# Optimization experiments

Hardware: AMD Instinct MI355X
Metric: run time of the kernel (lower is better)

Reference implementation:

```python
import jax, jax.numpy as jnp
import numpy as np

EMBED_DIM = 1024
NUM_HEADS = 16
HEAD_DIM = EMBED_DIM // NUM_HEADS


def setup_inputs() -> dict:
    key = jax.random.key(0)
    ks = jax.random.split(key, 9)
    B, S, D = 2, 2048, EMBED_DIM
    scale = 1.0 / np.sqrt(D)
    x = jax.random.normal(ks[0], (B, S, D), dtype=jnp.float32)
    Wq = jax.random.normal(ks[1], (D, D), dtype=jnp.float32) * scale
    Wk = jax.random.normal(ks[2], (D, D), dtype=jnp.float32) * scale
    Wv = jax.random.normal(ks[3], (D, D), dtype=jnp.float32) * scale
    Wo = jax.random.normal(ks[4], (D, D), dtype=jnp.float32) * scale
    bq = jnp.zeros((D,), jnp.float32)
    bk = jnp.zeros((D,), jnp.float32)
    bv = jnp.zeros((D,), jnp.float32)
    bo = jnp.zeros((D,), jnp.float32)
    return {"x": x, "Wq": Wq, "bq": bq, "Wk": Wk, "bk": bk,
            "Wv": Wv, "bv": bv, "Wo": Wo, "bo": bo}


def reference(x, Wq, bq, Wk, bk, Wv, bv, Wo, bo):
    B, S, D = x.shape
    H, Dh = NUM_HEADS, HEAD_DIM
    # QKV projections -> [B, H, S, Dh]
    q = (x @ Wq + bq).reshape(B, S, H, Dh).transpose(0, 2, 1, 3)
    k = (x @ Wk + bk).reshape(B, S, H, Dh).transpose(0, 2, 1, 3)
    v = (x @ Wv + bv).reshape(B, S, H, Dh).transpose(0, 2, 1, 3)
    # scores [B, H, S, S], scaled by sqrt(head_dim)
    scores = jnp.einsum('bhqd,bhkd->bhqk', q, k) / jnp.sqrt(jnp.float32(Dh))
    attn = jax.nn.softmax(scores, axis=-1)
    out = jnp.einsum('bhqk,bhkd->bhqd', attn, v)  # [B, H, S, Dh]
    out = out.transpose(0, 2, 1, 3).reshape(B, S, D)
    return out @ Wo + bo
```

## Files before the change

kernel.cpp:

```cpp
#include <hip/hip_runtime.h>
#include <hip/hip_bf16.h>

typedef short bf16x8 __attribute__((ext_vector_type(8)));
typedef float f32x4 __attribute__((ext_vector_type(4)));
typedef unsigned uint2v __attribute__((ext_vector_type(2)));

#define MFMA16(a, b, c) __builtin_amdgcn_mfma_f32_16x16x32_bf16((a), (b), (c), 0, 0, 0)

#if __has_builtin(__builtin_amdgcn_exp2f)
#define EXP2(x) __builtin_amdgcn_exp2f(x)
#else
#define EXP2(x) exp2f(x)
#endif

static constexpr int B_ = 2, S_ = 2048, D_ = 1024, H_ = 16, DH = 64;
static constexpr int M_ = B_ * S_;
static constexpr int K_ = D_;
static constexpr float kQS = 0.18033688011112042f;

static __device__ __forceinline__ ushort f2bf(float f) {
    __hip_bfloat16 h = __float2bfloat16(f);
    return *reinterpret_cast<ushort*>(&h);
}
static __device__ __forceinline__ float bf2f(ushort u) {
    __hip_bfloat16 h;
    *reinterpret_cast<ushort*>(&h) = u;
    return __bfloat162float(h);
}

static __device__ __forceinline__ void gload16(const ushort* g, ushort* l) {
    __builtin_amdgcn_global_load_lds((const __attribute__((address_space(1))) void*)g,
                                     (__attribute__((address_space(3))) void*)l, 16, 0, 0);
}

static __device__ __forceinline__ unsigned pkbf(float lo, float hi) {
    return __builtin_amdgcn_perm(__builtin_bit_cast(unsigned, hi),
                                 __builtin_bit_cast(unsigned, lo), 0x07060302u);
}

__global__ __launch_bounds__(256) void prep5(const float* __restrict__ x,
                                             const float* __restrict__ W0,
                                             const float* __restrict__ W1,
                                             const float* __restrict__ W2,
                                             const float* __restrict__ W3,
                                             ushort* __restrict__ xb,
                                             ushort* __restrict__ T0,
                                             ushort* __restrict__ T1,
                                             ushort* __restrict__ T2,
                                             ushort* __restrict__ T3) {
    int z = blockIdx.z;
    int tx = threadIdx.x, ty = threadIdx.y;
    int t = ty * 32 + tx;
    if (z == 4) {
        int blk = blockIdx.y * 32 + blockIdx.x;
#pragma unroll
        for (int k = 0; k < 4; k++) {
            int i = blk * 1024 + k * 256 + t;
            float4 v = reinterpret_cast<const float4*>(x)[i];
            ushort4 o;
            o.x = f2bf(v.x); o.y = f2bf(v.y); o.z = f2bf(v.z); o.w = f2bf(v.w);
            reinterpret_cast<ushort4*>(xb)[i] = o;
        }
        return;
    }
    __shared__ float tile[32][33];
    const float* W = (z == 0) ? W0 : (z == 1) ? W1 : (z == 2) ? W2 : W3;
    ushort* T = (z == 0) ? T0 : (z == 1) ? T1 : (z == 2) ? T2 : T3;
    float sc = (z == 0) ? kQS : 1.0f;
    int bx = blockIdx.x, by = blockIdx.y;
#pragma unroll
    for (int i = 0; i < 4; i++)
        tile[ty + i * 8][tx] = W[(by * 32 + ty + i * 8) * D_ + bx * 32 + tx];
    __syncthreads();
#pragma unroll
    for (int i = 0; i < 4; i++)
        T[(bx * 32 + ty + i * 8) * K_ + by * 32 + tx] = f2bf(tile[tx][ty + i * 8] * sc);
}

template <int MODE, int TN>
__global__ __launch_bounds__(256, 3) void gemm128(const ushort* __restrict__ A,
                                                  const ushort* __restrict__ Wt,
                                                  const float* __restrict__ bias_q,
                                                  const float* __restrict__ bias_k,
                                                  const float* __restrict__ bias_v,
                                                  ushort* __restrict__ Qb,
                                                  ushort* __restrict__ Kb,
                                                  ushort* __restrict__ Vtb,
                                                  float* __restrict__ outf) {
    constexpr int NJ = TN / 32;
    __shared__ __align__(16) ushort As[128 * 32];
    __shared__ __align__(16) ushort Bs[TN * 32];

    int m0 = blockIdx.x * 128;
    int n0 = blockIdx.y * TN;
    int t = threadIdx.x;
    int lane = t & 63, w = t >> 6;
    int ln = lane & 15, lq = lane >> 4;
    int wm = (w >> 1) * 64, wn = (w & 1) * (TN / 2);

    int c0 = t, c1 = t + 256;
    const ushort* Ag0 = A + (size_t)(m0 + (c0 >> 2)) * K_ + (c0 & 3) * 8;
    const ushort* Ag1 = A + (size_t)(m0 + (c1 >> 2)) * K_ + (c1 & 3) * 8;
    const ushort* Bg0 = Wt + (size_t)(n0 + (c0 >> 2)) * K_ + (c0 & 3) * 8;
    const ushort* Bg1 = Wt + (size_t)(n0 + (c1 >> 2)) * K_ + (c1 & 3) * 8;
    ushort* Al0 = As + c0 * 8;
    ushort* Al1 = As + c1 * 8;
    ushort* Bl0 = Bs + c0 * 8;
    ushort* Bl1 = Bs + c1 * 8;

    const bool swp = (MODE == 1) || (n0 < 2048);

    f32x4 acc[4][NJ];
#pragma unroll
    for (int i = 0; i < 4; i++)
#pragma unroll
        for (int j = 0; j < NJ; j++) acc[i][j] = f32x4{0.f, 0.f, 0.f, 0.f};

    if (swp) {
        for (int k0 = 0; k0 < K_; k0 += 32) {
            gload16(Ag0 + k0, Al0);
            gload16(Ag1 + k0, Al1);
            gload16(Bg0 + k0, Bl0);
            if (TN == 128) gload16(Bg1 + k0, Bl1);
            __syncthreads();
            bf16x8 af[4], bfr[NJ];
#pragma unroll
            for (int i = 0; i < 4; i++)
                af[i] = *reinterpret_cast<const bf16x8*>(As + (wm + i * 16 + ln) * 32 + lq * 8);
#pragma unroll
            for (int j = 0; j < NJ; j++)
                bfr[j] = *reinterpret_cast<const bf16x8*>(Bs + (wn + j * 16 + ln) * 32 + lq * 8);
#pragma unroll
            for (int i = 0; i < 4; i++)
#pragma unroll
                for (int j = 0; j < NJ; j++)
                    acc[i][j] = MFMA16(bfr[j], af[i], acc[i][j]);
            __syncthreads();
        }
    } else {
        for (int k0 = 0; k0 < K_; k0 += 32) {
            gload16(Ag0 + k0, Al0);
            gload16(Ag1 + k0, Al1);
            gload16(Bg0 + k0, Bl0);
            if (TN == 128) gload16(Bg1 + k0, Bl1);
            __syncthreads();
            bf16x8 af[4], bfr[NJ];
#pragma unroll
            for (int i = 0; i < 4; i++)
                af[i] = *reinterpret_cast<const bf16x8*>(As + (wm + i * 16 + ln) * 32 + lq * 8);
#pragma unroll
            for (int j = 0; j < NJ; j++)
                bfr[j] = *reinterpret_cast<const bf16x8*>(Bs + (wn + j * 16 + ln) * 32 + lq * 8);
#pragma unroll
            for (int i = 0; i < 4; i++)
#pragma unroll
                for (int j = 0; j < NJ; j++)
                    acc[i][j] = MFMA16(af[i], bfr[j], acc[i][j]);
            __syncthreads();
        }
    }

    if (MODE == 1) {
#pragma unroll
        for (int j = 0; j < NJ; j++) {
            int nb = n0 + wn + j * 16 + lq * 4;
            float4 bv4 = *reinterpret_cast<const float4*>(bias_q + nb);
#pragma unroll
            for (int i = 0; i < 4; i++) {
                int m = m0 + wm + i * 16 + ln;
                float4 o;
                o.x = acc[i][j][0] + bv4.x;
                o.y = acc[i][j][1] + bv4.y;
                o.z = acc[i][j][2] + bv4.z;
                o.w = acc[i][j][3] + bv4.w;
                *reinterpret_cast<float4*>(outf + (size_t)m * D_ + nb) = o;
            }
        }
    } else if (n0 < 2048) {
        int which = n0 >> 10;
        const float* bp = which ? bias_k : bias_q;
        ushort* dst = which ? Kb : Qb;
        float bsc = which ? 1.0f : kQS;
#pragma unroll
        for (int j = 0; j < NJ; j++) {
            int nb = ((n0 + wn + j * 16) & 1023) + lq * 4;
            int h = nb >> 6, dhb = nb & 63;
            float4 bv4 = *reinterpret_cast<const float4*>(bp + nb);
            bv4.x *= bsc; bv4.y *= bsc; bv4.z *= bsc; bv4.w *= bsc;
#pragma unroll
            for (int i = 0; i < 4; i++) {
                int m = m0 + wm + i * 16 + ln;
                int b = m >> 11, s = m & 2047;
                ushort4 o4;
                o4.x = f2bf(acc[i][j][0] + bv4.x);
                o4.y = f2bf(acc[i][j][1] + bv4.y);
                o4.z = f2bf(acc[i][j][2] + bv4.z);
                o4.w = f2bf(acc[i][j][3] + bv4.w);
                *reinterpret_cast<ushort4*>(dst + (((size_t)(b * H_ + h) * S_) + s) * DH + dhb) = o4;
            }
        }
    } else {
#pragma unroll
        for (int j = 0; j < NJ; j++) {
            int n = n0 + wn + j * 16 + ln;
            int nn = n & 1023, h = nn >> 6, dh = nn & 63;
            float bv = bias_v[nn];
#pragma unroll
            for (int i = 0; i < 4; i++) {
                int m = m0 + wm + i * 16 + lq * 4;
                int b = m >> 11, s0 = m & 2047;
                ushort4 o4;
                o4.x = f2bf(acc[i][j][0] + bv);
                o4.y = f2bf(acc[i][j][1] + bv);
                o4.z = f2bf(acc[i][j][2] + bv);
                o4.w = f2bf(acc[i][j][3] + bv);
                *reinterpret_cast<ushort4*>(Vtb + (((size_t)(b * H_ + h) * DH) + dh) * S_ + s0) = o4;
            }
        }
    }
}

__global__ __launch_bounds__(256, 4) void attn128s(const ushort* __restrict__ Q,
                                                   const ushort* __restrict__ K,
                                                   const ushort* __restrict__ Vt,
                                                   ushort* __restrict__ O1,
                                                   ushort* __restrict__ O2,
                                                   float* __restrict__ L) {
    __shared__ __align__(16) ushort Kl[512 * 8];
    __shared__ __align__(16) ushort Vl[512 * 8];
    __shared__ __align__(16) ushort Pl[4][2][16 * 72];

    int bid = blockIdx.x;
    int half = bid >> 9;
    int rem = bid & 511;
    int qb = rem & 15;
    int bh = rem >> 4;
    int t = threadIdx.x;
    int lane = t & 63, w = t >> 6;
    int ln = lane & 15, lq = lane >> 4;
    int q0 = qb * 128 + w * 32;

    const ushort* Qp = Q + (size_t)bh * S_ * DH;
    const ushort* Kp = K + (size_t)bh * S_ * DH + (size_t)half * 1024 * DH;
    const ushort* Vp = Vt + (size_t)bh * DH * S_ + (size_t)half * 1024;

    bf16x8 qf[2][2];
#pragma unroll
    for (int tl = 0; tl < 2; tl++) {
        const ushort* qp = Qp + (q0 + tl * 16 + ln) * DH + lq * 8;
        qf[tl][0] = *reinterpret_cast<const bf16x8*>(qp);
        qf[tl][1] = *reinterpret_cast<const bf16x8*>(qp + 32);
    }

    bf16x8 ones;
#pragma unroll
    for (int j = 0; j < 8; j++) ones[j] = (short)0x3F80;

    int c0 = t, c1 = t + 256;
    const ushort* Kg0 = Kp + (size_t)(c0 & 63) * DH + (c0 >> 6) * 8;
    const ushort* Kg1 = Kp + (size_t)(c1 & 63) * DH + (c1 >> 6) * 8;
    const ushort* Vg0 = Vp + (size_t)(c0 & 63) * S_ + (c0 >> 6) * 8;
    const ushort* Vg1 = Vp + (size_t)(c1 & 63) * S_ + (c1 >> 6) * 8;
    ushort* Kl0 = Kl + c0 * 8;
    ushort* Kl1 = Kl + c1 * 8;
    ushort* Vl0 = Vl + c0 * 8;
    ushort* Vl1 = Vl + c1 * 8;

    f32x4 o_acc[2][4];
    f32x4 l_acc[2];
#pragma unroll
    for (int tl = 0; tl < 2; tl++) {
        l_acc[tl] = f32x4{0.f, 0.f, 0.f, 0.f};
#pragma unroll
        for (int nt = 0; nt < 4; nt++) o_acc[tl][nt] = f32x4{0.f, 0.f, 0.f, 0.f};
    }

    for (int kt = 0; kt < 16; kt++) {
        int kb = kt * 64;
        gload16(Kg0 + (size_t)kb * DH, Kl0);
        gload16(Kg1 + (size_t)kb * DH, Kl1);
        gload16(Vg0 + kb, Vl0);
        gload16(Vg1 + kb, Vl1);
        __syncthreads();

        f32x4 sc[2][4];
#pragma unroll
        for (int nt = 0; nt < 4; nt++) {
            bf16x8 kf0 = *reinterpret_cast<const bf16x8*>(Kl + (lq * 64 + nt * 16 + ln) * 8);
            bf16x8 kf1 = *reinterpret_cast<const bf16x8*>(Kl + ((4 + lq) * 64 + nt * 16 + ln) * 8);
#pragma unroll
            for (int tl = 0; tl < 2; tl++) {
                f32x4 c = {0.f, 0.f, 0.f, 0.f};
                c = MFMA16(kf0, qf[tl][0], c);
                c = MFMA16(kf1, qf[tl][1], c);
                sc[tl][nt] = c;
            }
        }
#pragma unroll
        for (int tl = 0; tl < 2; tl++)
#pragma unroll
            for (int nt = 0; nt < 4; nt++) {
                float p0 = EXP2(sc[tl][nt][0]);
                float p1 = EXP2(sc[tl][nt][1]);
                float p2 = EXP2(sc[tl][nt][2]);
                float p3 = EXP2(sc[tl][nt][3]);
                uint2v pk;
                pk.x = pkbf(p0, p1);
                pk.y = pkbf(p2, p3);
                *reinterpret_cast<uint2v*>(&Pl[w][tl][ln * 72 + nt * 16 + lq * 4]) = pk;
            }
        bf16x8 pf[2][2];
#pragma unroll
        for (int tl = 0; tl < 2; tl++) {
            pf[tl][0] = *reinterpret_cast<const bf16x8*>(&Pl[w][tl][ln * 72 + lq * 8]);
            pf[tl][1] = *reinterpret_cast<const bf16x8*>(&Pl[w][tl][ln * 72 + 32 + lq * 8]);
            l_acc[tl] = MFMA16(pf[tl][0], ones, l_acc[tl]);
            l_acc[tl] = MFMA16(pf[tl][1], ones, l_acc[tl]);
        }
#pragma unroll
        for (int nt = 0; nt < 4; nt++) {
            bf16x8 vf0 = *reinterpret_cast<const bf16x8*>(Vl + (lq * 64 + nt * 16 + ln) * 8);
            bf16x8 vf1 = *reinterpret_cast<const bf16x8*>(Vl + ((4 + lq) * 64 + nt * 16 + ln) * 8);
#pragma unroll
            for (int tl = 0; tl < 2; tl++) {
                o_acc[tl][nt] = MFMA16(pf[tl][0], vf0, o_acc[tl][nt]);
                o_acc[tl][nt] = MFMA16(pf[tl][1], vf1, o_acc[tl][nt]);
            }
        }
        __syncthreads();
    }

    ushort* Op = half ? O2 : O1;
    float* Lp = L + ((size_t)half * 32 + bh) * S_;
    int b = bh >> 4, h = bh & 15;
#pragma unroll
    for (int tl = 0; tl < 2; tl++) {
        float linv[4];
#pragma unroll
        for (int r = 0; r < 4; r++) {
            linv[r] = 1.0f / l_acc[tl][r];
            if (ln == 0) Lp[q0 + tl * 16 + lq * 4 + r] = l_acc[tl][r];
        }
#pragma unroll
        for (int nt = 0; nt < 4; nt++)
#pragma unroll
            for (int r = 0; r < 4; r++) {
                int s = q0 + tl * 16 + lq * 4 + r;
                Op[((b * S_ + s) * H_ + h) * DH + nt * 16 + ln] =
                    f2bf(o_acc[tl][nt][r] * linv[r]);
            }
    }
}

__global__ __launch_bounds__(256) void attn_comb(const ushort* __restrict__ O1,
                                                 const ushort* __restrict__ O2,
                                                 const float* __restrict__ L,
                                                 ushort* __restrict__ AO) {
    int i = blockIdx.x * 256 + threadIdx.x;
    int row = i >> 7;
    int col = (i & 127) * 8;
    int h = col >> 6;
    int b = row >> 11, s = row & 2047;
    int bh = b * 16 + h;
    float l1 = L[(size_t)bh * S_ + s];
    float l2 = L[((size_t)32 + bh) * S_ + s];
    float inv = 1.0f / (l1 + l2);
    float w1 = l1 * inv, w2 = l2 * inv;
    size_t off = (size_t)row * D_ + col;
    ushort4 a0 = reinterpret_cast<const ushort4*>(O1 + off)[0];
    ushort4 a1 = reinterpret_cast<const ushort4*>(O1 + off)[1];
    ushort4 b0 = reinterpret_cast<const ushort4*>(O2 + off)[0];
    ushort4 b1 = reinterpret_cast<const ushort4*>(O2 + off)[1];
    ushort4 o0, o1v;
    o0.x = f2bf(w1 * bf2f(a0.x) + w2 * bf2f(b0.x));
    o0.y = f2bf(w1 * bf2f(a0.y) + w2 * bf2f(b0.y));
    o0.z = f2bf(w1 * bf2f(a0.z) + w2 * bf2f(b0.z));
    o0.w = f2bf(w1 * bf2f(a0.w) + w2 * bf2f(b0.w));
    o1v.x = f2bf(w1 * bf2f(a1.x) + w2 * bf2f(b1.x));
    o1v.y = f2bf(w1 * bf2f(a1.y) + w2 * bf2f(b1.y));
    o1v.z = f2bf(w1 * bf2f(a1.z) + w2 * bf2f(b1.z));
    o1v.w = f2bf(w1 * bf2f(a1.w) + w2 * bf2f(b1.w));
    reinterpret_cast<ushort4*>(AO + off)[0] = o0;
    reinterpret_cast<ushort4*>(AO + off)[1] = o1v;
}

extern "C" void kernel_launch(void* const* d_in, const int* in_sizes, int n_in,
                              void* d_out, int out_size, void* d_ws, size_t ws_size,
                              hipStream_t stream) {
    const float* x  = (const float*)d_in[0];
    const float* Wq = (const float*)d_in[1];
    const float* bq = (const float*)d_in[2];
    const float* Wk = (const float*)d_in[3];
    const float* bk = (const float*)d_in[4];
    const float* Wv = (const float*)d_in[5];
    const float* bv = (const float*)d_in[6];
    const float* Wo = (const float*)d_in[7];
    const float* bo = (const float*)d_in[8];
    float* out = (float*)d_out;

    char* ws = (char*)d_ws;
    const size_t MB = 1024 * 1024;
    ushort* wtq = (ushort*)(ws + 0 * MB);
    ushort* wtk = (ushort*)(ws + 2 * MB);
    ushort* wtv = (ushort*)(ws + 4 * MB);
    ushort* wto = (ushort*)(ws + 6 * MB);
    ushort* xb  = (ushort*)(ws + 8 * MB);
    ushort* Qb  = (ushort*)(ws + 16 * MB);
    ushort* Kb  = (ushort*)(ws + 24 * MB);
    ushort* Vtb = (ushort*)(ws + 32 * MB);
    ushort* AO  = (ushort*)(ws + 40 * MB);
    ushort* O1  = (ushort*)(ws + 8 * MB);
    ushort* O2  = (ushort*)(ws + 48 * MB);
    float*  Lw  = (float*)(ws + 56 * MB);

    prep5<<<dim3(32, 32, 5), dim3(32, 8), 0, stream>>>(
        x, Wq, Wk, Wv, Wo, xb, wtq, wtk, wtv, wto);

    gemm128<0, 128><<<dim3(M_ / 128, 3072 / 128), 256, 0, stream>>>(
        xb, wtq, bq, bk, bv, Qb, Kb, Vtb, nullptr);

    attn128s<<<1024, 256, 0, stream>>>(Qb, Kb, Vtb, O1, O2, Lw);
    attn_comb<<<(M_ * D_ / 8) / 256, 256, 0, stream>>>(O1, O2, Lw, AO);

    gemm128<1, 64><<<dim3(M_ / 128, D_ / 64), 256, 0, stream>>>(
        AO, wto, bo, nullptr, nullptr, nullptr, nullptr, nullptr, out);
}
```

Measured before the change: 198.8 us.

## Double GEMM K-step to 64 and use chunk-major LDS layout

The projection GEMM now stages 64 K-elements per iteration instead of 32. This halves the number of barrier pairs and global-load rounds per tile. The shared-memory layout switches to chunk-major (k-chunk by row), so fragment reads by consecutive lanes hit consecutive 16-byte slots and should avoid bank conflicts. The swap/no-swap branch moves inside the loop. LDS use doubles, which may reduce occupancy under the 3-blocks-per-CU launch bound.

```diff
diff --git a/kernel.cpp b/kernel.cpp
--- a/kernel.cpp
+++ b/kernel.cpp
@@ -88,8 +88,9 @@
                                                   ushort* __restrict__ Vtb,
                                                   float* __restrict__ outf) {
     constexpr int NJ = TN / 32;
-    __shared__ __align__(16) ushort As[128 * 32];
-    __shared__ __align__(16) ushort Bs[TN * 32];
+    constexpr int NBCH = TN * 8 / 256;
+    __shared__ __align__(16) ushort As[128 * 64];
+    __shared__ __align__(16) ushort Bs[TN * 64];
 
     int m0 = blockIdx.x * 128;
     int n0 = blockIdx.y * TN;
@@ -98,15 +99,22 @@
     int ln = lane & 15, lq = lane >> 4;
     int wm = (w >> 1) * 64, wn = (w & 1) * (TN / 2);
 
-    int c0 = t, c1 = t + 256;
-    const ushort* Ag0 = A + (size_t)(m0 + (c0 >> 2)) * K_ + (c0 & 3) * 8;
-    const ushort* Ag1 = A + (size_t)(m0 + (c1 >> 2)) * K_ + (c1 & 3) * 8;
-    const ushort* Bg0 = Wt + (size_t)(n0 + (c0 >> 2)) * K_ + (c0 & 3) * 8;
-    const ushort* Bg1 = Wt + (size_t)(n0 + (c1 >> 2)) * K_ + (c1 & 3) * 8;
-    ushort* Al0 = As + c0 * 8;
-    ushort* Al1 = As + c1 * 8;
-    ushort* Bl0 = Bs + c0 * 8;
-    ushort* Bl1 = Bs + c1 * 8;
+    const ushort* Ag[4];
+    ushort* Al[4];
+#pragma unroll
+    for (int u = 0; u < 4; u++) {
+        int c = t + u * 256;
+        Ag[u] = A + (size_t)(m0 + (c & 127)) * K_ + (c >> 7) * 8;
+        Al[u] = As + c * 8;
+    }
+    const ushort* Bg[NBCH];
+    ushort* Bl[NBCH];
+#pragma unroll
+    for (int u = 0; u < NBCH; u++) {
+        int c = t + u * 256;
+        Bg[u] = Wt + (size_t)(n0 + (c & (TN - 1))) * K_ + (c / TN) * 8;
+        Bl[u] = Bs + c * 8;
+    }
 
     const bool swp = (MODE == 1) || (n0 < 2048);
 
@@ -116,48 +124,38 @@
 #pragma unroll
         for (int j = 0; j < NJ; j++) acc[i][j] = f32x4{0.f, 0.f, 0.f, 0.f};
 
-    if (swp) {
-        for (int k0 = 0; k0 < K_; k0 += 32) {
-            gload16(Ag0 + k0, Al0);
-            gload16(Ag1 + k0, Al1);
-            gload16(Bg0 + k0, Bl0);
-            if (TN == 128) gload16(Bg1 + k0, Bl1);
-            __syncthreads();
+    for (int k0 = 0; k0 < K_; k0 += 64) {
+#pragma unroll
+        for (int u = 0; u < 4; u++) gload16(Ag[u] + k0, Al[u]);
+#pragma unroll
+        for (int u = 0; u < NBCH; u++) gload16(Bg[u] + k0, Bl[u]);
+        __syncthreads();
+#pragma unroll
+        for (int kk = 0; kk < 2; kk++) {
             bf16x8 af[4], bfr[NJ];
 #pragma unroll
             for (int i = 0; i < 4; i++)
-                af[i] = *reinterpret_cast<const bf16x8*>(As + (wm + i * 16 + ln) * 32 + lq * 8);
+                af[i] = *reinterpret_cast<const bf16x8*>(
+                    As + ((kk * 4 + lq) * 128 + wm + i * 16 + ln) * 8);
 #pragma unroll
             for (int j = 0; j < NJ; j++)
-                bfr[j] = *reinterpret_cast<const bf16x8*>(Bs + (wn + j * 16 + ln) * 32 + lq * 8);
-#pragma unroll
-            for (int i = 0; i < 4; i++)
-#pragma unroll
-                for (int j = 0; j < NJ; j++)
-                    acc[i][j] = MFMA16(bfr[j], af[i], acc[i][j]);
-            __syncthreads();
-        }
-    } else {
-        for (int k0 = 0; k0 < K_; k0 += 32) {
-            gload16(Ag0 + k0, Al0);
-            gload16(Ag1 + k0, Al1);
-            gload16(Bg0 + k0, Bl0);
-            if (TN == 128) gload16(Bg1 + k0, Bl1);
-            __syncthreads();
-            bf16x8 af[4], bfr[NJ];
-#pragma unroll
-            for (int i = 0; i < 4; i++)
-                af[i] = *reinterpret_cast<const bf16x8*>(As + (wm + i * 16 + ln) * 32 + lq * 8);
-#pragma unroll
-            for (int j = 0; j < NJ; j++)
-                bfr[j] = *reinterpret_cast<const bf16x8*>(Bs + (wn + j * 16 + ln) * 32 + lq * 8);
-#pragma unroll
-            for (int i = 0; i < 4; i++)
-#pragma unroll
-                for (int j = 0; j < NJ; j++)
-                    acc[i][j] = MFMA16(af[i], bfr[j], acc[i][j]);
-            __syncthreads();
-        }
+                bfr[j] = *reinterpret_cast<const bf16x8*>(
+                    Bs + ((kk * 4 + lq) * TN + wn + j * 16 + ln) * 8);
+            if (swp) {
+#pragma unroll
+                for (int i = 0; i < 4; i++)
+#pragma unroll
+                    for (int j = 0; j < NJ; j++)
+                        acc[i][j] = MFMA16(bfr[j], af[i], acc[i][j]);
+            } else {
+#pragma unroll
+                for (int i = 0; i < 4; i++)
+#pragma unroll
+                    for (int j = 0; j < NJ; j++)
+                        acc[i][j] = MFMA16(af[i], bfr[j], acc[i][j]);
+            }
+        }
+        __syncthreads();
     }
 
     if (MODE == 1) {
```

Result: slower. 254.1 us (+27.8%).
